# Kernel tuning notes

Hardware: AMD Instinct MI355X
Metric: run time of the kernel (lower is better)

## Reference

```python
import jax, jax.numpy as jnp
import numpy as np

N = 10000      # nodes
E = 320000     # directed edges (self-loops added in reference)
F_IN = 78      # atom features
D = 128        # embed_dim per head
H = 4          # heads in layer 1
G = 64         # graphs in batch
NEG_SLOPE = 0.2


def setup_inputs() -> dict:
    key = jax.random.key(0)
    ks = jax.random.split(key, 12)
    s = 0.05
    return {
        "x": jax.random.normal(ks[0], (N, F_IN), dtype=jnp.float32),
        "edge_index": jax.random.randint(ks[1], (2, E), 0, N, dtype=jnp.int64),
        "batch": jnp.sort(jax.random.randint(ks[2], (N,), 0, G, dtype=jnp.int64)),
        "Wl1": jax.random.normal(ks[3], (F_IN, H * D), dtype=jnp.float32) * s,
        "bl1": jnp.zeros((H * D,), jnp.float32),
        "Wr1": jax.random.normal(ks[4], (F_IN, H * D), dtype=jnp.float32) * s,
        "br1": jnp.zeros((H * D,), jnp.float32),
        "att1": jax.random.normal(ks[5], (H, D), dtype=jnp.float32) * s,
        "bias1": jnp.zeros((H * D,), jnp.float32),
        "Wl2": jax.random.normal(ks[6], (H * D, D), dtype=jnp.float32) * s,
        "bl2": jnp.zeros((D,), jnp.float32),
        "Wr2": jax.random.normal(ks[7], (H * D, D), dtype=jnp.float32) * s,
        "br2": jnp.zeros((D,), jnp.float32),
        "att2": jax.random.normal(ks[8], (1, D), dtype=jnp.float32) * s,
        "bias2": jnp.zeros((D,), jnp.float32),
    }


def gatv2_conv(x, src, dst, Wl, bl, Wr, br, att, bias, heads, out_ch):
    # x: [N, Fin]; src/dst: [Etot] (self-loops already included)
    n = x.shape[0]
    x_l = (x @ Wl + bl).reshape(n, heads, out_ch)  # source transform
    x_r = (x @ Wr + br).reshape(n, heads, out_ch)  # target transform
    # per-edge GATv2 score: att . LeakyReLU(x_l[src] + x_r[dst])
    e = x_l[src] + x_r[dst]                                   # [E, H, C]
    e = jnp.where(e > 0, e, NEG_SLOPE * e)                    # leaky_relu 0.2
    logits = jnp.einsum('ehc,hc->eh', e, att)                 # [E, H]
    # segment softmax over destination nodes (every node has a self-loop)
    seg_max = jax.ops.segment_max(logits, dst, num_segments=n)
    alpha = jnp.exp(logits - seg_max[dst])
    seg_sum = jax.ops.segment_sum(alpha, dst, num_segments=n)
    alpha = alpha / seg_sum[dst]                              # [E, H]
    # weighted scatter-sum aggregation of source features
    msg = alpha[:, :, None] * x_l[src]                        # [E, H, C]
    out = jax.ops.segment_sum(msg, dst, num_segments=n)       # [N, H, C]
    return out.reshape(n, heads * out_ch) + bias


def reference(x, edge_index, batch, Wl1, bl1, Wr1, br1, att1, bias1,
              Wl2, bl2, Wr2, br2, att2, bias2):
    n = x.shape[0]
    loops = jnp.arange(n, dtype=edge_index.dtype)
    src = jnp.concatenate([edge_index[0], loops])
    dst = jnp.concatenate([edge_index[1], loops])

    h = gatv2_conv(x, src, dst, Wl1, bl1, Wr1, br1, att1, bias1, H, D)
    h = jax.nn.elu(h)  # dropout: identity in eval mode
    h = gatv2_conv(h, src, dst, Wl2, bl2, Wr2, br2, att2, bias2, 1, D)
    h = jax.nn.elu(h)

    # global mean pool over graphs
    sums = jax.ops.segment_sum(h, batch, num_segments=G)          # [G, D]
    cnts = jax.ops.segment_sum(jnp.ones((n,), h.dtype), batch, num_segments=G)
    return sums / jnp.maximum(cnts, 1.0)[:, None]
```

## Files before the change

kernel.cpp:

```cpp
#include <hip/hip_runtime.h>
#include <hip/hip_fp16.h>
#include <math.h>

#define FIN 78
#define HD1 512
#define D2  128
#define KP1 40

typedef _Float16 f16x2 __attribute__((ext_vector_type(2)));
union U2H { unsigned u; f16x2 h; __half2 hh; };
__device__ __forceinline__ f16x2 u2h(unsigned u) { U2H x; x.u = u; return x.h; }
union V16 { uint4 u4; f16x2 h[4]; };

__device__ __forceinline__ float elu(float x) { return x > 0.f ? x : expf(x) - 1.f; }

__global__ void cvtW_k(const float* __restrict__ Wl1, const float* __restrict__ Wr1,
                       const float* __restrict__ Wl2, const float* __restrict__ Wr2,
                       unsigned* __restrict__ Wt1, unsigned* __restrict__ Wt2)
{
    int idx = blockIdx.x * 256 + threadIdx.x;
    if (idx < 1024 * KP1) {
        int k2 = idx >> 10, col = idx & 1023;
        const float* W = (col < HD1) ? Wl1 : Wr1;
        int c = (col < HD1) ? col : col - HD1;
        float w0 = (2 * k2     < FIN) ? W[(2 * k2)     * HD1 + c] : 0.f;
        float w1 = (2 * k2 + 1 < FIN) ? W[(2 * k2 + 1) * HD1 + c] : 0.f;
        U2H x; x.h = (f16x2){(_Float16)w0, (_Float16)w1};
        Wt1[idx] = x.u;
    } else if (idx < 1024 * KP1 + 256 * 256) {
        int j = idx - 1024 * KP1;
        int k2 = j >> 8, col = j & 255;
        const float* W = (col < D2) ? Wl2 : Wr2;
        int c = (col < D2) ? col : col - D2;
        float w0 = W[(2 * k2) * D2 + c], w1 = W[(2 * k2 + 1) * D2 + c];
        U2H x; x.h = (f16x2){(_Float16)w0, (_Float16)w1};
        Wt2[j] = x.u;
    }
}

__global__ __launch_bounds__(256, 4)
void gemm1_k(const float* __restrict__ x, const unsigned* __restrict__ Wt1,
             const float* __restrict__ bl, const float* __restrict__ br,
             __half* __restrict__ xl, __half* __restrict__ xr, int N)
{
    __shared__ unsigned hs[16][KP1];
    int row0 = blockIdx.x * 16;
    int t = threadIdx.x;
    for (int idx = t; idx < 16 * KP1; idx += 256) {
        int r = idx / KP1, k2 = idx - r * KP1;
        int row = row0 + r;
        float lo = 0.f, hi = 0.f;
        if (row < N) {
            lo = (2 * k2     < FIN) ? x[(size_t)row * FIN + 2 * k2]     : 0.f;
            hi = (2 * k2 + 1 < FIN) ? x[(size_t)row * FIN + 2 * k2 + 1] : 0.f;
        }
        U2H p; p.h = (f16x2){(_Float16)lo, (_Float16)hi};
        hs[r][k2] = p.u;
    }
    __syncthreads();

    float acc[16][4];
#pragma unroll
    for (int r = 0; r < 16; ++r)
        { acc[r][0]=0.f; acc[r][1]=0.f; acc[r][2]=0.f; acc[r][3]=0.f; }

    for (int k2 = 0; k2 < KP1; ++k2) {
        const unsigned* wp = Wt1 + (size_t)k2 * 1024;
        unsigned w0 = wp[t], w1 = wp[t + 256], w2 = wp[t + 512], w3 = wp[t + 768];
#pragma unroll
        for (int r = 0; r < 16; ++r) {
            f16x2 xv = u2h(hs[r][k2]);
            acc[r][0] = __builtin_amdgcn_fdot2(xv, u2h(w0), acc[r][0], false);
            acc[r][1] = __builtin_amdgcn_fdot2(xv, u2h(w1), acc[r][1], false);
            acc[r][2] = __builtin_amdgcn_fdot2(xv, u2h(w2), acc[r][2], false);
            acc[r][3] = __builtin_amdgcn_fdot2(xv, u2h(w3), acc[r][3], false);
        }
    }

#pragma unroll
    for (int i = 0; i < 4; ++i) {
        int j = t + i * 256;
        bool isL = j < HD1;
        int col = isL ? j : j - HD1;
        float b = isL ? bl[col] : br[col];
        __half* outp = isL ? xl : xr;
        for (int r = 0; r < 16; ++r) {
            int row = row0 + r;
            if (row < N) outp[(size_t)row * HD1 + col] = __float2half(acc[r][i] + b);
        }
    }
}

__global__ __launch_bounds__(256, 4)
void gemm2_k(const __half* __restrict__ h, const unsigned* __restrict__ Wt,
             const float* __restrict__ bl, const float* __restrict__ br,
             __half* __restrict__ xl, __half* __restrict__ xr, int N)
{
    __shared__ unsigned hs[16][256];
    int row0 = blockIdx.x * 16;
    int t = threadIdx.x;
    for (int idx = t; idx < 16 * 64; idx += 256) {
        int r = idx >> 6, q = idx & 63;
        int row = row0 + r;
        uint4 val = make_uint4(0u, 0u, 0u, 0u);
        if (row < N) val = *(const uint4*)(h + (size_t)row * HD1 + q * 8);
        *(uint4*)&hs[r][q * 4] = val;
    }
    __syncthreads();

    int c = t & 127, rg = t >> 7;
    float acc[8][2];
#pragma unroll
    for (int r = 0; r < 8; ++r) { acc[r][0] = 0.f; acc[r][1] = 0.f; }

    for (int k2 = 0; k2 < 256; ++k2) {
        uint2 w01 = *(const uint2*)(Wt + (size_t)k2 * 256 + 2 * c);
        f16x2 w0 = u2h(w01.x), w1 = u2h(w01.y);
#pragma unroll
        for (int r = 0; r < 8; ++r) {
            f16x2 hv = u2h(hs[rg * 8 + r][k2]);
            acc[r][0] = __builtin_amdgcn_fdot2(hv, w0, acc[r][0], false);
            acc[r][1] = __builtin_amdgcn_fdot2(hv, w1, acc[r][1], false);
        }
    }

    if (c < 64) {
        int cc = 2 * c;
        float b0 = bl[cc], b1 = bl[cc + 1];
#pragma unroll
        for (int r = 0; r < 8; ++r) {
            int row = row0 + rg * 8 + r;
            if (row < N) {
                U2H o; o.h = (f16x2){(_Float16)(acc[r][0] + b0), (_Float16)(acc[r][1] + b1)};
                *(unsigned*)(xl + (size_t)row * D2 + cc) = o.u;
            }
        }
    } else {
        int cc = 2 * c - 128;
        float b0 = br[cc], b1 = br[cc + 1];
#pragma unroll
        for (int r = 0; r < 8; ++r) {
            int row = row0 + rg * 8 + r;
            if (row < N) {
                U2H o; o.h = (f16x2){(_Float16)(acc[r][0] + b0), (_Float16)(acc[r][1] + b1)};
                *(unsigned*)(xr + (size_t)row * D2 + cc) = o.u;
            }
        }
    }
}

__global__ void count_k(const int* __restrict__ ei, int E, int Etot, int* __restrict__ counts)
{
    int e = blockIdx.x * 256 + threadIdx.x;
    if (e >= Etot) return;
    int dst = (e < E) ? ei[E + e] : (e - E);
    atomicAdd(&counts[dst], 1);
}

__global__ void scan_k(const int* __restrict__ counts, int* __restrict__ row_ptr,
                       int* __restrict__ offs, int N)
{
    __shared__ int sdata[1024];
    int t = threadIdx.x;
    int chunk = (N + 1023) / 1024;
    int lo = t * chunk, hi = min(lo + chunk, N);
    int p = 0;
    for (int i = lo; i < hi; ++i) p += counts[i];
    sdata[t] = p;
    __syncthreads();
    for (int off = 1; off < 1024; off <<= 1) {
        int v = (t >= off) ? sdata[t - off] : 0;
        __syncthreads();
        sdata[t] += v;
        __syncthreads();
    }
    int run = sdata[t] - p;
    for (int i = lo; i < hi; ++i) { row_ptr[i] = run; offs[i] = run; run += counts[i]; }
    if (t == 1023) row_ptr[N] = sdata[1023];
}

__global__ void scatter_k(const int* __restrict__ ei, int E, int Etot,
                          int* __restrict__ offs, int* __restrict__ csr_src)
{
    int e = blockIdx.x * 256 + threadIdx.x;
    if (e >= Etot) return;
    int src, dst;
    if (e < E) { src = ei[e]; dst = ei[E + e]; } else { src = dst = e - E; }
    int pos = atomicAdd(&offs[dst], 1);
    csr_src[pos] = src;
}

__global__ __launch_bounds__(256, 8)
void fused1_k(const int* __restrict__ row_ptr, const int* __restrict__ csr_src,
              const __half* __restrict__ xl, const __half* __restrict__ xr,
              const float* __restrict__ att, const float* __restrict__ bias,
              __half* __restrict__ out)
{
    int v = blockIdx.x;
    int t = threadIdx.x;
    int w = t >> 6, lane = t & 63;
    int g = lane >> 4, sub = lane & 15;
    int base = row_ptr[v], deg = row_ptr[v + 1] - base;
    int c0 = (w << 7) + (sub << 3);

    V16 bb; bb.u4 = *(const uint4*)(xr + (size_t)v * HD1 + c0);
    f16x2 at_h[4];
    {
        float4 t0 = *(const float4*)(att + c0);
        float4 t1 = *(const float4*)(att + c0 + 4);
        at_h[0] = (f16x2){(_Float16)t0.x, (_Float16)t0.y};
        at_h[1] = (f16x2){(_Float16)t0.z, (_Float16)t0.w};
        at_h[2] = (f16x2){(_Float16)t1.x, (_Float16)t1.y};
        at_h[3] = (f16x2){(_Float16)t1.z, (_Float16)t1.w};
    }
    const f16x2 c02 = {(_Float16)0.2f, (_Float16)0.2f};

    float s = 0.f, a[8];
#pragma unroll
    for (int j = 0; j < 8; ++j) a[j] = 0.f;

    for (int i = g; i < deg; i += 4) {
        int src = csr_src[base + i];
        V16 af; af.u4 = *(const uint4*)(xl + (size_t)src * HD1 + c0);
        float p = 0.f;
#pragma unroll
        for (int j = 0; j < 4; ++j) {
            f16x2 th = af.h[j] + bb.h[j];
            f16x2 uh = __builtin_elementwise_max(th, th * c02);
            p = __builtin_amdgcn_fdot2(uh, at_h[j], p, false);
        }
#pragma unroll
        for (int off = 1; off < 16; off <<= 1) p += __shfl_xor(p, off);
        float e = __expf(p);
        s += e;
#pragma unroll
        for (int j = 0; j < 4; ++j) {
            a[2*j]   += e * (float)af.h[j].x;
            a[2*j+1] += e * (float)af.h[j].y;
        }
    }
    s += __shfl_xor(s, 16); s += __shfl_xor(s, 32);
#pragma unroll
    for (int j = 0; j < 8; ++j) { a[j] += __shfl_xor(a[j], 16); a[j] += __shfl_xor(a[j], 32); }

    if (g == 0) {
        float rs = 1.f / s;
        V16 pk;
#pragma unroll
        for (int j = 0; j < 4; ++j)
            pk.h[j] = (f16x2){(_Float16)elu(a[2*j]   * rs + bias[c0 + 2*j]),
                              (_Float16)elu(a[2*j+1] * rs + bias[c0 + 2*j+1])};
        *(uint4*)(out + (size_t)v * HD1 + c0) = pk.u4;
    }
}

__global__ __launch_bounds__(256, 8)
void fused2_k(const int* __restrict__ row_ptr, const int* __restrict__ csr_src,
              const __half* __restrict__ xl, const __half* __restrict__ xr,
              const float* __restrict__ att, const float* __restrict__ bias,
              float* __restrict__ out, int N)
{
    int t = threadIdx.x;
    int w = t >> 6, lane = t & 63;
    int v = blockIdx.x * 4 + w;
    if (v >= N) return;
    int g = lane >> 4, sub = lane & 15;
    int base = row_ptr[v], deg = row_ptr[v + 1] - base;
    int c0 = sub << 3;

    V16 bb; bb.u4 = *(const uint4*)(xr + (size_t)v * D2 + c0);
    f16x2 at_h[4];
    {
        float4 t0 = *(const float4*)(att + c0);
        float4 t1 = *(const float4*)(att + c0 + 4);
        at_h[0] = (f16x2){(_Float16)t0.x, (_Float16)t0.y};
        at_h[1] = (f16x2){(_Float16)t0.z, (_Float16)t0.w};
        at_h[2] = (f16x2){(_Float16)t1.x, (_Float16)t1.y};
        at_h[3] = (f16x2){(_Float16)t1.z, (_Float16)t1.w};
    }
    const f16x2 c02 = {(_Float16)0.2f, (_Float16)0.2f};

    float s = 0.f, a[8];
#pragma unroll
    for (int j = 0; j < 8; ++j) a[j] = 0.f;

    for (int i = g; i < deg; i += 4) {
        int src = csr_src[base + i];
        V16 af; af.u4 = *(const uint4*)(xl + (size_t)src * D2 + c0);
        float p = 0.f;
#pragma unroll
        for (int j = 0; j < 4; ++j) {
            f16x2 th = af.h[j] + bb.h[j];
            f16x2 uh = __builtin_elementwise_max(th, th * c02);
            p = __builtin_amdgcn_fdot2(uh, at_h[j], p, false);
        }
#pragma unroll
        for (int off = 1; off < 16; off <<= 1) p += __shfl_xor(p, off);
        float e = __expf(p);
        s += e;
#pragma unroll
        for (int j = 0; j < 4; ++j) {
            a[2*j]   += e * (float)af.h[j].x;
            a[2*j+1] += e * (float)af.h[j].y;
        }
    }
    s += __shfl_xor(s, 16); s += __shfl_xor(s, 32);
#pragma unroll
    for (int j = 0; j < 8; ++j) { a[j] += __shfl_xor(a[j], 16); a[j] += __shfl_xor(a[j], 32); }

    if (g == 0) {
        float rs = 1.f / s;
        float o[8];
#pragma unroll
        for (int j = 0; j < 8; ++j) o[j] = elu(a[j] * rs + bias[c0 + j]);
        size_t ob = (size_t)v * D2 + c0;
        *(float4*)(out + ob)     = make_float4(o[0], o[1], o[2], o[3]);
        *(float4*)(out + ob + 4) = make_float4(o[4], o[5], o[6], o[7]);
    }
}

__global__ void pool2_k(const int* __restrict__ batch, const float* __restrict__ h,
                        float* __restrict__ out, int N)
{
    __shared__ float part[D2];
    int g = blockIdx.x;
    int t = threadIdx.x;
    int c = t & 127, half = t >> 7;
    int lo = 0, hi = N;
    while (lo < hi) { int m = (lo + hi) >> 1; if (batch[m] < g) lo = m + 1; else hi = m; }
    int lo2 = lo, hi2 = N;
    while (lo2 < hi2) { int m = (lo2 + hi2) >> 1; if (batch[m] < g + 1) lo2 = m + 1; else hi2 = m; }
    float acc = 0.f;
    for (int v = lo + half; v < lo2; v += 2)
        acc += h[(size_t)v * D2 + c];
    if (half == 1) part[c] = acc;
    __syncthreads();
    if (half == 0)
        out[(size_t)g * D2 + c] = (acc + part[c]) / fmaxf((float)(lo2 - lo), 1.f);
}

extern "C" void kernel_launch(void* const* d_in, const int* in_sizes, int n_in,
                              void* d_out, int out_size, void* d_ws, size_t ws_size,
                              hipStream_t stream)
{
    const float* x    = (const float*)d_in[0];
    const int*   ei   = (const int*)d_in[1];
    const int*   batch= (const int*)d_in[2];
    const float* Wl1  = (const float*)d_in[3];
    const float* bl1  = (const float*)d_in[4];
    const float* Wr1  = (const float*)d_in[5];
    const float* br1  = (const float*)d_in[6];
    const float* att1 = (const float*)d_in[7];
    const float* bias1= (const float*)d_in[8];
    const float* Wl2  = (const float*)d_in[9];
    const float* bl2  = (const float*)d_in[10];
    const float* Wr2  = (const float*)d_in[11];
    const float* br2  = (const float*)d_in[12];
    const float* att2 = (const float*)d_in[13];
    const float* bias2= (const float*)d_in[14];
    float* out = (float*)d_out;

    int N    = in_sizes[2];
    int E    = in_sizes[1] / 2;
    int Etot = E + N;
    int G    = out_size / D2;

    char* ws = (char*)d_ws;
    size_t off = 0;
    auto alloc = [&](size_t bytes) -> void* {
        void* p = ws + off;
        off = (off + bytes + 255) & ~(size_t)255;
        return p;
    };
    __half*   xl1h   = (__half*)alloc((size_t)N * HD1 * 2);
    __half*   xr1h   = (__half*)alloc((size_t)N * HD1 * 2);
    __half*   h1h    = (__half*)alloc((size_t)N * HD1 * 2);
    __half*   xl2h   = (__half*)alloc((size_t)N * D2 * 2);
    __half*   xr2h   = (__half*)alloc((size_t)N * D2 * 2);
    float*    h2     = (float*)alloc((size_t)N * D2 * 4);
    unsigned* Wt1    = (unsigned*)alloc((size_t)1024 * KP1 * 4);
    unsigned* Wt2    = (unsigned*)alloc((size_t)256 * 256 * 4);
    int*      counts = (int*)alloc((size_t)(N + 1) * 4);
    int*      offs   = (int*)alloc((size_t)(N + 1) * 4);
    int*      row_ptr= (int*)alloc((size_t)(N + 1) * 4);
    int*      csr_src= (int*)alloc((size_t)Etot * 4);

    int wtot = 1024 * KP1 + 256 * 256;
    (void)hipMemsetAsync(counts, 0, (size_t)(N + 1) * 4, stream);
    cvtW_k<<<(wtot + 255) / 256, 256, 0, stream>>>(Wl1, Wr1, Wl2, Wr2, Wt1, Wt2);
    gemm1_k<<<(N + 15) / 16, 256, 0, stream>>>(x, Wt1, bl1, br1, xl1h, xr1h, N);
    count_k<<<(Etot + 255) / 256, 256, 0, stream>>>(ei, E, Etot, counts);
    scan_k<<<1, 1024, 0, stream>>>(counts, row_ptr, offs, N);
    scatter_k<<<(Etot + 255) / 256, 256, 0, stream>>>(ei, E, Etot, offs, csr_src);
    fused1_k<<<N, 256, 0, stream>>>(row_ptr, csr_src, xl1h, xr1h, att1, bias1, h1h);
    gemm2_k<<<(N + 15) / 16, 256, 0, stream>>>(h1h, Wt2, bl2, br2, xl2h, xr2h, N);
    fused2_k<<<(N + 3) / 4, 256, 0, stream>>>(row_ptr, csr_src, xl2h, xr2h, att2, bias2, h2, N);
    pool2_k<<<G, 256, 0, stream>>>(batch, h2, out, N);
}
```

Baseline: 242.4 us.

## Merge weight conversion with edge counting and prefetch next neighbor row in aggregation

The weight fp16 conversion and the destination-degree counting now run as one launch, with blocks split by index, which removes one kernel launch and its dependency gap. Both fused GAT aggregation kernels also software-prefetch the next neighbor's feature vector (index plus 16-byte load) before working on the current one, so the gather latency overlaps the score and exp math. This costs extra registers per thread and may lower occupancy.

```diff
diff --git a/kernel.cpp b/kernel.cpp
--- a/kernel.cpp
+++ b/kernel.cpp
@@ -14,27 +14,36 @@
 
 __device__ __forceinline__ float elu(float x) { return x > 0.f ? x : expf(x) - 1.f; }
 
-__global__ void cvtW_k(const float* __restrict__ Wl1, const float* __restrict__ Wr1,
+__global__ void prep_k(const float* __restrict__ Wl1, const float* __restrict__ Wr1,
                        const float* __restrict__ Wl2, const float* __restrict__ Wr2,
-                       unsigned* __restrict__ Wt1, unsigned* __restrict__ Wt2)
-{
-    int idx = blockIdx.x * 256 + threadIdx.x;
-    if (idx < 1024 * KP1) {
-        int k2 = idx >> 10, col = idx & 1023;
-        const float* W = (col < HD1) ? Wl1 : Wr1;
-        int c = (col < HD1) ? col : col - HD1;
-        float w0 = (2 * k2     < FIN) ? W[(2 * k2)     * HD1 + c] : 0.f;
-        float w1 = (2 * k2 + 1 < FIN) ? W[(2 * k2 + 1) * HD1 + c] : 0.f;
-        U2H x; x.h = (f16x2){(_Float16)w0, (_Float16)w1};
-        Wt1[idx] = x.u;
-    } else if (idx < 1024 * KP1 + 256 * 256) {
-        int j = idx - 1024 * KP1;
-        int k2 = j >> 8, col = j & 255;
-        const float* W = (col < D2) ? Wl2 : Wr2;
-        int c = (col < D2) ? col : col - D2;
-        float w0 = W[(2 * k2) * D2 + c], w1 = W[(2 * k2 + 1) * D2 + c];
-        U2H x; x.h = (f16x2){(_Float16)w0, (_Float16)w1};
-        Wt2[j] = x.u;
+                       unsigned* __restrict__ Wt1, unsigned* __restrict__ Wt2,
+                       const int* __restrict__ ei, int E, int Etot,
+                       int* __restrict__ counts, int nWB)
+{
+    if ((int)blockIdx.x < nWB) {
+        int idx = blockIdx.x * 256 + threadIdx.x;
+        if (idx < 1024 * KP1) {
+            int k2 = idx >> 10, col = idx & 1023;
+            const float* W = (col < HD1) ? Wl1 : Wr1;
+            int c = (col < HD1) ? col : col - HD1;
+            float w0 = (2 * k2     < FIN) ? W[(2 * k2)     * HD1 + c] : 0.f;
+            float w1 = (2 * k2 + 1 < FIN) ? W[(2 * k2 + 1) * HD1 + c] : 0.f;
+            U2H x; x.h = (f16x2){(_Float16)w0, (_Float16)w1};
+            Wt1[idx] = x.u;
+        } else if (idx < 1024 * KP1 + 256 * 256) {
+            int j = idx - 1024 * KP1;
+            int k2 = j >> 8, col = j & 255;
+            const float* W = (col < D2) ? Wl2 : Wr2;
+            int c = (col < D2) ? col : col - D2;
+            float w0 = W[(2 * k2) * D2 + c], w1 = W[(2 * k2 + 1) * D2 + c];
+            U2H x; x.h = (f16x2){(_Float16)w0, (_Float16)w1};
+            Wt2[j] = x.u;
+        }
+    } else {
+        int e = (blockIdx.x - nWB) * 256 + threadIdx.x;
+        if (e >= Etot) return;
+        int dst = (e < E) ? ei[E + e] : (e - E);
+        atomicAdd(&counts[dst], 1);
     }
 }
 
@@ -147,14 +156,6 @@
             }
         }
     }
-}
-
-__global__ void count_k(const int* __restrict__ ei, int E, int Etot, int* __restrict__ counts)
-{
-    int e = blockIdx.x * 256 + threadIdx.x;
-    if (e >= Etot) return;
-    int dst = (e < E) ? ei[E + e] : (e - E);
-    atomicAdd(&counts[dst], 1);
 }
 
 __global__ void scan_k(const int* __restrict__ counts, int* __restrict__ row_ptr,
@@ -219,9 +220,15 @@
 #pragma unroll
     for (int j = 0; j < 8; ++j) a[j] = 0.f;
 
+    V16 afn;
+    if (g < deg)
+        afn.u4 = *(const uint4*)(xl + (size_t)csr_src[base + g] * HD1 + c0);
+
     for (int i = g; i < deg; i += 4) {
-        int src = csr_src[base + i];
-        V16 af; af.u4 = *(const uint4*)(xl + (size_t)src * HD1 + c0);
+        V16 af = afn;
+        int inext = i + 4;
+        if (inext < deg)
+            afn.u4 = *(const uint4*)(xl + (size_t)csr_src[base + inext] * HD1 + c0);
         float p = 0.f;
 #pragma unroll
         for (int j = 0; j < 4; ++j) {
@@ -284,9 +291,15 @@
 #pragma unroll
     for (int j = 0; j < 8; ++j) a[j] = 0.f;
 
+    V16 afn;
+    if (g < deg)
+        afn.u4 = *(const uint4*)(xl + (size_t)csr_src[base + g] * D2 + c0);
+
     for (int i = g; i < deg; i += 4) {
-        int src = csr_src[base + i];
-        V16 af; af.u4 = *(const uint4*)(xl + (size_t)src * D2 + c0);
+        V16 af = afn;
+        int inext = i + 4;
+        if (inext < deg)
+            afn.u4 = *(const uint4*)(xl + (size_t)csr_src[base + inext] * D2 + c0);
         float p = 0.f;
 #pragma unroll
         for (int j = 0; j < 4; ++j) {
@@ -386,10 +399,11 @@
     int*      csr_src= (int*)alloc((size_t)Etot * 4);
 
     int wtot = 1024 * KP1 + 256 * 256;
+    int nWB  = (wtot + 255) / 256;
+    int nCB  = (Etot + 255) / 256;
     (void)hipMemsetAsync(counts, 0, (size_t)(N + 1) * 4, stream);
-    cvtW_k<<<(wtot + 255) / 256, 256, 0, stream>>>(Wl1, Wr1, Wl2, Wr2, Wt1, Wt2);
+    prep_k<<<nWB + nCB, 256, 0, stream>>>(Wl1, Wr1, Wl2, Wr2, Wt1, Wt2, ei, E, Etot, counts, nWB);
     gemm1_k<<<(N + 15) / 16, 256, 0, stream>>>(x, Wt1, bl1, br1, xl1h, xr1h, N);
-    count_k<<<(Etot + 255) / 256, 256, 0, stream>>>(ei, E, Etot, counts);
     scan_k<<<1, 1024, 0, stream>>>(counts, row_ptr, offs, N);
     scatter_k<<<(Etot + 255) / 256, 256, 0, stream>>>(ei, E, Etot, offs, csr_src);
     fused1_k<<<N, 256, 0, stream>>>(row_ptr, csr_src, xl1h, xr1h, att1, bias1, h1h);
```

After: 234.2 us, median of 2. -3.4%, faster.
